# Kernel tuning notes

Hardware: AMD Instinct MI355X
Metric: run time of the kernel (lower is better)

## Reference

```python
import jax, jax.numpy as jnp
import numpy as np

B, S, D = 32, 1, 2048
H, KVH, HD = 16, 4, 128
MAXS = 4096
EPS = 1e-5
NREP = H // KVH  # GQA repeat factor = 4
FF = 4 * D
POS = 4095  # decode position (start_pos)


def setup_inputs() -> dict:
    key = jax.random.key(0)
    ks = jax.random.split(key, 12)
    sc = lambda d: 1.0 / np.sqrt(d)
    # RoPE angles for the current token position, [S, HD//2]
    inv_freq = 1.0 / (10000.0 ** (np.arange(0, HD, 2, dtype=np.float32) / HD))
    ang = (POS + np.arange(S, dtype=np.float32))[:, None] * inv_freq[None, :]
    return {
        "x": jax.random.normal(ks[0], (B, S, D), jnp.float32),
        "cos": jnp.asarray(np.cos(ang), jnp.float32),
        "sin": jnp.asarray(np.sin(ang), jnp.float32),
        "k_cache": jax.random.normal(ks[1], (B, MAXS, KVH, HD), jnp.float32),
        "v_cache": jax.random.normal(ks[2], (B, MAXS, KVH, HD), jnp.float32),
        "w_rms_attn": jnp.ones((D,), jnp.float32),
        "wq": jax.random.normal(ks[3], (D, D), jnp.float32) * sc(D),
        "wk": jax.random.normal(ks[4], (D, KVH * HD), jnp.float32) * sc(D),
        "wv": jax.random.normal(ks[5], (D, KVH * HD), jnp.float32) * sc(D),
        "wo": jax.random.normal(ks[6], (D, D), jnp.float32) * sc(D),
        "w_rms_ffn": jnp.ones((D,), jnp.float32),
        "w1": jax.random.normal(ks[7], (D, FF), jnp.float32) * sc(D),
        "w2": jax.random.normal(ks[8], (D, FF), jnp.float32) * sc(D),
        "w3": jax.random.normal(ks[9], (FF, D), jnp.float32) * sc(FF),
        "start_pos": POS,
    }


def _rmsnorm(x, g):
    return x * g * jax.lax.rsqrt(jnp.mean(x * x, axis=-1, keepdims=True) + EPS)


def _rope(x, cos, sin):
    # x: [B, S, h, HD]; complex rotation on (even, odd) pairs
    xr = x.reshape(*x.shape[:-1], HD // 2, 2)
    x0, x1 = xr[..., 0], xr[..., 1]
    c = cos[None, :, None, :]
    s = sin[None, :, None, :]
    r0 = x0 * c - x1 * s
    r1 = x0 * s + x1 * c
    return jnp.stack([r0, r1], axis=-1).reshape(x.shape)


def reference(x, cos, sin, k_cache, v_cache, w_rms_attn, wq, wk, wv, wo,
              w_rms_ffn, w1, w2, w3, start_pos):
    xa = _rmsnorm(x, w_rms_attn)
    xq = (xa @ wq).reshape(B, S, H, HD)
    xk = (xa @ wk).reshape(B, S, KVH, HD)
    xv = (xa @ wv).reshape(B, S, KVH, HD)
    # Source applies RoPE to K and V (not Q) -- reproduced faithfully.
    xk = _rope(xk, cos, sin)
    xv = _rope(xv, cos, sin)
    kc = jax.lax.dynamic_update_slice(k_cache, xk, (0, start_pos, 0, 0))
    vc = jax.lax.dynamic_update_slice(v_cache, xv, (0, start_pos, 0, 0))
    klen = start_pos + S
    keys = jnp.repeat(kc[:, :klen], NREP, axis=2)   # [B, klen, H, HD]
    vals = jnp.repeat(vc[:, :klen], NREP, axis=2)
    att = jnp.einsum('bqhd,bkhd->bhqk', xq, keys) * (HD ** -0.5)
    att = jax.nn.softmax(att, axis=-1)
    y = jnp.einsum('bhqk,bkhd->bqhd', att, vals).reshape(B, S, D)
    h = x + y @ wo
    xf = _rmsnorm(h, w_rms_ffn)
    return h + (jax.nn.silu(xf @ w1) * (xf @ w2)) @ w3
```

## Files before the change

kernel.cpp:

```cpp
#include <hip/hip_runtime.h>
#include <math.h>

#define BB 32
#define DD 2048
#define NKVH 4
#define HDIM 128
#define MAXS 4096
#define FFD 8192
#define POS 4095
#define EPSV 1e-5f
#define SCALE 0.08838834764831845f
#define ASPLIT 32
#define SPOS 128

#define OFF_QT   0u
#define OFF_KT   65536u
#define OFF_VT   81920u
#define OFF_G1   98304u
#define OFF_G2   360448u
#define ZERO_N   622592u
#define OFF_XAT  622592u
#define OFF_RK   688128u
#define OFF_RV   704512u
#define OFF_PML  720896u
#define OFF_PACC 753664u
#define OFF_YT   2850816u
#define OFF_H    2916352u
#define OFF_XFT  2981888u

#define REP32(M) M(0) M(1) M(2) M(3) M(4) M(5) M(6) M(7) M(8) M(9) M(10) M(11) M(12) M(13) M(14) M(15) M(16) M(17) M(18) M(19) M(20) M(21) M(22) M(23) M(24) M(25) M(26) M(27) M(28) M(29) M(30) M(31)
#define REP32A(M,X) M(0,X) M(1,X) M(2,X) M(3,X) M(4,X) M(5,X) M(6,X) M(7,X) M(8,X) M(9,X) M(10,X) M(11,X) M(12,X) M(13,X) M(14,X) M(15,X) M(16,X) M(17,X) M(18,X) M(19,X) M(20,X) M(21,X) M(22,X) M(23,X) M(24,X) M(25,X) M(26,X) M(27,X) M(28,X) M(29,X) M(30,X) M(31,X)

#define DECLA(i) float a##i = 0.f;
#define FMA1(i,k) a##i = fmaf(ap[(k)*32 + (i)], w##k, a##i);
#define STORET(i) tl[i] = a##i;
#define ATOMN(i) atomicAdd(C + (size_t)(i)*N + n, a##i);

template<int N, int CH, bool TOUT>
__device__ __forceinline__ void gemv_body(const float* __restrict__ At,
                                          const float* __restrict__ W,
                                          float* __restrict__ C, int colblk,
                                          float* tile) {
    int tid = (int)threadIdx.x;
    int n = colblk * 256 + tid;
    int d0 = blockIdx.y * CH;
    const float* Wp = W + (size_t)d0 * N + n;
    const float* ap = At + (size_t)d0 * 32;
    REP32(DECLA)
#pragma unroll 4
    for (int dd = 0; dd < CH; dd += 4) {
        float w0 = Wp[0];
        float w1 = Wp[(size_t)N];
        float w2 = Wp[(size_t)N * 2];
        float w3 = Wp[(size_t)N * 3];
        REP32A(FMA1, 0)
        REP32A(FMA1, 1)
        REP32A(FMA1, 2)
        REP32A(FMA1, 3)
        Wp += (size_t)N * 4;
        ap += 128;
    }
    if constexpr (TOUT) {
        float* tl = tile + tid * 33;
        REP32(STORET)
        __syncthreads();
        float* cb = C + (size_t)colblk * 256 * 32;
#pragma unroll
        for (int i = 0; i < 32; ++i) {
            int f = i * 256 + tid;
            atomicAdd(cb + f, tile[(f >> 5) * 33 + (f & 31)]);
        }
    } else {
        REP32(ATOMN)
    }
}

template<int N, int CH, bool TOUT>
__global__ __launch_bounds__(256) void gemv32_kernel(const float* __restrict__ At,
                                                     const float* __restrict__ W,
                                                     float* __restrict__ C) {
    if constexpr (TOUT) {
        __shared__ float tile[256 * 33];
        gemv_body<N, CH, true>(At, W, C, blockIdx.x, tile);
    } else {
        gemv_body<N, CH, false>(At, W, C, blockIdx.x, nullptr);
    }
}

template<int N, int CH, int HALF>
__global__ __launch_bounds__(256) void gemv32_dual_kernel(const float* __restrict__ At,
        const float* __restrict__ W0, const float* __restrict__ W1,
        float* __restrict__ C0, float* __restrict__ C1) {
    __shared__ float tile[256 * 33];
    int bx = blockIdx.x;
    if (bx < HALF) gemv_body<N, CH, true>(At, W0, C0, bx, tile);
    else           gemv_body<N, CH, true>(At, W1, C1, bx - HALF, tile);
}

__global__ void zero_kernel(float* __restrict__ p) {
    p[blockIdx.x * 256 + threadIdx.x] = 0.f;
}

__global__ void rmsnorm_kernel(const float* __restrict__ in, const float* __restrict__ g,
                               float* __restrict__ outT, float* __restrict__ cpy) {
    int b = blockIdx.x;
    int tid = threadIdx.x;
    const float* row = in + b * DD;
    float v[8];
    float ss = 0.f;
#pragma unroll
    for (int i = 0; i < 8; ++i) { v[i] = row[tid + i * 256]; ss += v[i] * v[i]; }
#pragma unroll
    for (int off = 32; off; off >>= 1) ss += __shfl_xor(ss, off);
    __shared__ float red[4];
    if ((tid & 63) == 0) red[tid >> 6] = ss;
    __syncthreads();
    ss = red[0] + red[1] + red[2] + red[3];
    float scale = rsqrtf(ss * (1.f / DD) + EPSV);
#pragma unroll
    for (int i = 0; i < 8; ++i) {
        int idx = tid + i * 256;
        outT[(size_t)idx * 32 + b] = v[i] * g[idx] * scale;
        if (cpy) cpy[b * DD + idx] = v[i];
    }
}

__global__ void rope_kernel(const float* __restrict__ kT, const float* __restrict__ vT,
                            const float* __restrict__ cosb, const float* __restrict__ sinb,
                            float* __restrict__ rk, float* __restrict__ rv) {
    int idx = blockIdx.x * 256 + threadIdx.x;
    int b = idx >> 8, rem = idx & 255;
    int kvh = rem >> 6, i = rem & 63;
    float c = cosb[i], s = sinb[i];
    int col = kvh * HDIM + 2 * i;
    float k0 = kT[(size_t)col * 32 + b], k1 = kT[(size_t)(col + 1) * 32 + b];
    float v0 = vT[(size_t)col * 32 + b], v1 = vT[(size_t)(col + 1) * 32 + b];
    int o = (b * NKVH + kvh) * HDIM + 2 * i;
    rk[o] = k0 * c - k1 * s; rk[o + 1] = k0 * s + k1 * c;
    rv[o] = v0 * c - v1 * s; rv[o + 1] = v0 * s + v1 * c;
}

__global__ __launch_bounds__(256) void attn_partial_kernel(
    const float* __restrict__ qT, const float* __restrict__ kc, const float* __restrict__ vc,
    const float* __restrict__ rk, const float* __restrict__ rv,
    float* __restrict__ pml, float* __restrict__ pacc) {
    int bid = blockIdx.x;
    int split = bid & 31, b = bid >> 5;
    int tid = threadIdx.x;
    int kvh = (tid >> 5) & 3;
    int c = tid & 31;
    int hi = tid >> 7;
    __shared__ float p_s[16][SPOS];
    __shared__ float red[128][17];

    float4 q4[4];
#pragma unroll
    for (int h = 0; h < 4; ++h) {
        int col = (kvh * 4 + h) * HDIM + c * 4;
        q4[h].x = qT[(size_t)(col + 0) * 32 + b];
        q4[h].y = qT[(size_t)(col + 1) * 32 + b];
        q4[h].z = qT[(size_t)(col + 2) * 32 + b];
        q4[h].w = qT[(size_t)(col + 3) * 32 + b];
    }
    int t0 = split * SPOS;
    const float* kbase = kc + (size_t)(b * MAXS + t0) * (NKVH * HDIM);
    const float* vbase = vc + (size_t)(b * MAXS + t0) * (NKVH * HDIM);

#define QK_BODY(SRC, POSL)                                                      \
    {                                                                           \
        float4 kk = *(const float4*)(SRC);                                      \
        float r0 = kk.x * q4[0].x + kk.y * q4[0].y + kk.z * q4[0].z + kk.w * q4[0].w; \
        float r1 = kk.x * q4[1].x + kk.y * q4[1].y + kk.z * q4[1].z + kk.w * q4[1].w; \
        float r2 = kk.x * q4[2].x + kk.y * q4[2].y + kk.z * q4[2].z + kk.w * q4[2].w; \
        float r3 = kk.x * q4[3].x + kk.y * q4[3].y + kk.z * q4[3].z + kk.w * q4[3].w; \
        _Pragma("unroll")                                                       \
        for (int m = 1; m < 32; m <<= 1) {                                      \
            r0 += __shfl_xor(r0, m); r1 += __shfl_xor(r1, m);                   \
            r2 += __shfl_xor(r2, m); r3 += __shfl_xor(r3, m);                   \
        }                                                                       \
        if (c == 0) {                                                           \
            p_s[kvh * 4 + 0][POSL] = r0 * SCALE;                                \
            p_s[kvh * 4 + 1][POSL] = r1 * SCALE;                                \
            p_s[kvh * 4 + 2][POSL] = r2 * SCALE;                                \
            p_s[kvh * 4 + 3][POSL] = r3 * SCALE;                                \
        }                                                                       \
    }

#pragma unroll 8
    for (int iter = 0; iter < 63; ++iter) {
        QK_BODY(kbase + iter * 1024 + tid * 4, iter * 2 + hi)
    }
    {
        int posl = 126 + hi;
        const float* src = (t0 + posl == POS)
            ? rk + (size_t)(b * NKVH + kvh) * HDIM + c * 4
            : kbase + 63 * 1024 + tid * 4;
        QK_BODY(src, posl)
    }
    __syncthreads();

    {
        int w = tid >> 6, lane = tid & 63;
#pragma unroll
        for (int hh = 0; hh < 4; ++hh) {
            int h = w * 4 + hh;
            float e0 = p_s[h][lane], e1 = p_s[h][lane + 64];
            float m = fmaxf(e0, e1);
#pragma unroll
            for (int off = 32; off; off >>= 1) m = fmaxf(m, __shfl_xor(m, off));
            e0 = __expf(e0 - m); e1 = __expf(e1 - m);
            p_s[h][lane] = e0; p_s[h][lane + 64] = e1;
            float l = e0 + e1;
#pragma unroll
            for (int off = 32; off; off >>= 1) l += __shfl_xor(l, off);
            if (lane == 0) {
                int idx = ((b * ASPLIT + split) * 16 + h) * 2;
                pml[idx] = m; pml[idx + 1] = l;
            }
        }
    }
    __syncthreads();

    float4 a0 = {0, 0, 0, 0}, a1 = a0, a2 = a0, a3 = a0;
#define PV_BODY(SRC, POSL)                                                      \
    {                                                                           \
        float4 vv = *(const float4*)(SRC);                                      \
        float p0 = p_s[kvh * 4 + 0][POSL], p1 = p_s[kvh * 4 + 1][POSL];         \
        float p2 = p_s[kvh * 4 + 2][POSL], p3 = p_s[kvh * 4 + 3][POSL];         \
        a0.x = fmaf(p0, vv.x, a0.x); a0.y = fmaf(p0, vv.y, a0.y);               \
        a0.z = fmaf(p0, vv.z, a0.z); a0.w = fmaf(p0, vv.w, a0.w);               \
        a1.x = fmaf(p1, vv.x, a1.x); a1.y = fmaf(p1, vv.y, a1.y);               \
        a1.z = fmaf(p1, vv.z, a1.z); a1.w = fmaf(p1, vv.w, a1.w);               \
        a2.x = fmaf(p2, vv.x, a2.x); a2.y = fmaf(p2, vv.y, a2.y);               \
        a2.z = fmaf(p2, vv.z, a2.z); a2.w = fmaf(p2, vv.w, a2.w);               \
        a3.x = fmaf(p3, vv.x, a3.x); a3.y = fmaf(p3, vv.y, a3.y);               \
        a3.z = fmaf(p3, vv.z, a3.z); a3.w = fmaf(p3, vv.w, a3.w);               \
    }
#pragma unroll 8
    for (int iter = 0; iter < 63; ++iter) {
        PV_BODY(vbase + iter * 1024 + tid * 4, iter * 2 + hi)
    }
    {
        int posl = 126 + hi;
        const float* src = (t0 + posl == POS)
            ? rv + (size_t)(b * NKVH + kvh) * HDIM + c * 4
            : vbase + 63 * 1024 + tid * 4;
        PV_BODY(src, posl)
    }
    if (tid >= 128) {
        float* r = &red[tid - 128][0];
        *(float4*)(r + 0) = a0; *(float4*)(r + 4) = a1;
        *(float4*)(r + 8) = a2; *(float4*)(r + 12) = a3;
    }
    __syncthreads();
    if (tid < 128) {
        const float* r = &red[tid][0];
        a0.x += r[0];  a0.y += r[1];  a0.z += r[2];  a0.w += r[3];
        a1.x += r[4];  a1.y += r[5];  a1.z += r[6];  a1.w += r[7];
        a2.x += r[8];  a2.y += r[9];  a2.z += r[10]; a2.w += r[11];
        a3.x += r[12]; a3.y += r[13]; a3.z += r[14]; a3.w += r[15];
        size_t base = ((size_t)(b * ASPLIT + split) * 16 + kvh * 4) * HDIM + c * 4;
        *(float4*)(pacc + base + 0 * HDIM) = a0;
        *(float4*)(pacc + base + 1 * HDIM) = a1;
        *(float4*)(pacc + base + 2 * HDIM) = a2;
        *(float4*)(pacc + base + 3 * HDIM) = a3;
    }
}

__global__ void attn_combine_kernel(const float* __restrict__ pml,
                                    const float* __restrict__ pacc, float* __restrict__ yT) {
    int bid = blockIdx.x;
    int b = bid >> 4, h = bid & 15;
    int d = threadIdx.x;
    float M = -INFINITY;
#pragma unroll 8
    for (int s = 0; s < ASPLIT; ++s)
        M = fmaxf(M, pml[((b * ASPLIT + s) * 16 + h) * 2]);
    float denom = 0.f, acc = 0.f;
#pragma unroll 4
    for (int s = 0; s < ASPLIT; ++s) {
        int idx = (b * ASPLIT + s) * 16 + h;
        float e = __expf(pml[idx * 2] - M);
        denom += pml[idx * 2 + 1] * e;
        acc += e * pacc[(size_t)idx * HDIM + d];
    }
    yT[(size_t)(h * HDIM + d) * 32 + b] = acc / denom;
}

__global__ void silu_mul_kernel(float* __restrict__ g1, const float* __restrict__ g2) {
    int i = blockIdx.x * 256 + threadIdx.x;
    float a = g1[i], bb = g2[i];
    g1[i] = a * bb / (1.f + __expf(-a));
}

extern "C" void kernel_launch(void* const* d_in, const int* in_sizes, int n_in,
                              void* d_out, int out_size, void* d_ws, size_t ws_size,
                              hipStream_t stream) {
    (void)in_sizes; (void)n_in; (void)out_size; (void)ws_size;
    const float* x    = (const float*)d_in[0];
    const float* cosb = (const float*)d_in[1];
    const float* sinb = (const float*)d_in[2];
    const float* kc   = (const float*)d_in[3];
    const float* vc   = (const float*)d_in[4];
    const float* wra  = (const float*)d_in[5];
    const float* wq   = (const float*)d_in[6];
    const float* wk   = (const float*)d_in[7];
    const float* wv   = (const float*)d_in[8];
    const float* wo   = (const float*)d_in[9];
    const float* wrf  = (const float*)d_in[10];
    const float* w1   = (const float*)d_in[11];
    const float* w2   = (const float*)d_in[12];
    const float* w3   = (const float*)d_in[13];
    float* out = (float*)d_out;
    float* ws  = (float*)d_ws;

    float* qT   = ws + OFF_QT;
    float* kT   = ws + OFF_KT;
    float* vT   = ws + OFF_VT;
    float* g1T  = ws + OFF_G1;
    float* g2T  = ws + OFF_G2;
    float* xaT  = ws + OFF_XAT;
    float* rk   = ws + OFF_RK;
    float* rv   = ws + OFF_RV;
    float* pml  = ws + OFF_PML;
    float* pacc = ws + OFF_PACC;
    float* yT   = ws + OFF_YT;
    float* h    = ws + OFF_H;
    float* xfT  = ws + OFF_XFT;

    zero_kernel<<<ZERO_N / 256, 256, 0, stream>>>(ws);

    rmsnorm_kernel<<<32, 256, 0, stream>>>(x, wra, xaT, h);
    gemv32_kernel<2048, 32, true><<<dim3(8, 64), 256, 0, stream>>>(xaT, wq, qT);
    gemv32_dual_kernel<512, 32, 2><<<dim3(4, 64), 256, 0, stream>>>(xaT, wk, wv, kT, vT);
    rope_kernel<<<32, 256, 0, stream>>>(kT, vT, cosb, sinb, rk, rv);
    attn_partial_kernel<<<1024, 256, 0, stream>>>(qT, kc, vc, rk, rv, pml, pacc);
    attn_combine_kernel<<<512, 128, 0, stream>>>(pml, pacc, yT);
    gemv32_kernel<2048, 32, false><<<dim3(8, 64), 256, 0, stream>>>(yT, wo, h);
    rmsnorm_kernel<<<32, 256, 0, stream>>>(h, wrf, xfT, out);
    gemv32_dual_kernel<8192, 128, 32><<<dim3(64, 16), 256, 0, stream>>>(xfT, w1, w2, g1T, g2T);
    silu_mul_kernel<<<1024, 256, 0, stream>>>(g1T, g2T);
    gemv32_kernel<2048, 128, false><<<dim3(8, 64), 256, 0, stream>>>(g1T, w3, out);
}
```

Baseline: 337.1 us.

## Stage KV cache tiles into LDS with async double-buffered loads in attention

```diff
diff --git a/kernel.cpp b/kernel.cpp
--- a/kernel.cpp
+++ b/kernel.cpp
@@ -27,6 +27,14 @@
 #define OFF_YT   2850816u
 #define OFF_H    2916352u
 #define OFF_XFT  2981888u
+#define OFF_KFIX 3047424u
+#define OFF_VFIX 3309568u
+
+#define VM_WAIT8 asm volatile("s_waitcnt vmcnt(8)" ::: "memory")
+#define VM_WAIT0 asm volatile("s_waitcnt vmcnt(0)" ::: "memory")
+#define LG_WAIT0 asm volatile("s_waitcnt lgkmcnt(0)" ::: "memory")
+#define SCHED0   __builtin_amdgcn_sched_barrier(0)
+#define SBAR     __builtin_amdgcn_s_barrier()
 
 #define REP32(M) M(0) M(1) M(2) M(3) M(4) M(5) M(6) M(7) M(8) M(9) M(10) M(11) M(12) M(13) M(14) M(15) M(16) M(17) M(18) M(19) M(20) M(21) M(22) M(23) M(24) M(25) M(26) M(27) M(28) M(29) M(30) M(31)
 #define REP32A(M,X) M(0,X) M(1,X) M(2,X) M(3,X) M(4,X) M(5,X) M(6,X) M(7,X) M(8,X) M(9,X) M(10,X) M(11,X) M(12,X) M(13,X) M(14,X) M(15,X) M(16,X) M(17,X) M(18,X) M(19,X) M(20,X) M(21,X) M(22,X) M(23,X) M(24,X) M(25,X) M(26,X) M(27,X) M(28,X) M(29,X) M(30,X) M(31,X)
@@ -140,131 +148,116 @@
     rv[o] = v0 * c - v1 * s; rv[o + 1] = v0 * s + v1 * c;
 }
 
-__global__ __launch_bounds__(256) void attn_partial_kernel(
-    const float* __restrict__ qT, const float* __restrict__ kc, const float* __restrict__ vc,
-    const float* __restrict__ rk, const float* __restrict__ rv,
+__global__ void fixlast_kernel(const float* __restrict__ kc, const float* __restrict__ vc,
+                               const float* __restrict__ rk, const float* __restrict__ rv,
+                               float* __restrict__ kfix, float* __restrict__ vfix) {
+    int idx = blockIdx.x * 256 + threadIdx.x;
+    int b = idx >> 13, rem = idx & 8191;
+    int pos = rem >> 9, col = rem & 511;
+    int gpos = 4080 + pos;
+    float kv, vv;
+    if (gpos == POS) {
+        kv = rk[b * 512 + col]; vv = rv[b * 512 + col];
+    } else {
+        size_t o = ((size_t)(b * MAXS + gpos)) * 512 + col;
+        kv = kc[o]; vv = vc[o];
+    }
+    kfix[idx] = kv; vfix[idx] = vv;
+}
+
+__global__ __launch_bounds__(256, 2) void attn_stage_kernel(
+    const float* __restrict__ qn, const float* __restrict__ kc, const float* __restrict__ vc,
+    const float* __restrict__ kfix, const float* __restrict__ vfix,
     float* __restrict__ pml, float* __restrict__ pacc) {
-    int bid = blockIdx.x;
-    int split = bid & 31, b = bid >> 5;
-    int tid = threadIdx.x;
-    int kvh = (tid >> 5) & 3;
-    int c = tid & 31;
-    int hi = tid >> 7;
-    __shared__ float p_s[16][SPOS];
-    __shared__ float red[128][17];
-
-    float4 q4[4];
-#pragma unroll
-    for (int h = 0; h < 4; ++h) {
-        int col = (kvh * 4 + h) * HDIM + c * 4;
-        q4[h].x = qT[(size_t)(col + 0) * 32 + b];
-        q4[h].y = qT[(size_t)(col + 1) * 32 + b];
-        q4[h].z = qT[(size_t)(col + 2) * 32 + b];
-        q4[h].w = qT[(size_t)(col + 3) * 32 + b];
-    }
+    int split = blockIdx.x & 31, b = blockIdx.x >> 5;
+    int tid = threadIdx.x, lane = tid & 63, wv = tid >> 6;
+    __shared__ float kbuf[2][8192];
+    __shared__ float p_s[128][16];
+    int qpos = tid >> 4, qhead = tid & 15;
+    int qr = qpos * 4 + (qhead >> 2);
+    int vh = tid >> 4, c16 = tid & 15, vkvh = vh >> 2;
     int t0 = split * SPOS;
-    const float* kbase = kc + (size_t)(b * MAXS + t0) * (NKVH * HDIM);
-    const float* vbase = vc + (size_t)(b * MAXS + t0) * (NKVH * HDIM);
-
-#define QK_BODY(SRC, POSL)                                                      \
-    {                                                                           \
-        float4 kk = *(const float4*)(SRC);                                      \
-        float r0 = kk.x * q4[0].x + kk.y * q4[0].y + kk.z * q4[0].z + kk.w * q4[0].w; \
-        float r1 = kk.x * q4[1].x + kk.y * q4[1].y + kk.z * q4[1].z + kk.w * q4[1].w; \
-        float r2 = kk.x * q4[2].x + kk.y * q4[2].y + kk.z * q4[2].z + kk.w * q4[2].w; \
-        float r3 = kk.x * q4[3].x + kk.y * q4[3].y + kk.z * q4[3].z + kk.w * q4[3].w; \
-        _Pragma("unroll")                                                       \
-        for (int m = 1; m < 32; m <<= 1) {                                      \
-            r0 += __shfl_xor(r0, m); r1 += __shfl_xor(r1, m);                   \
-            r2 += __shfl_xor(r2, m); r3 += __shfl_xor(r3, m);                   \
-        }                                                                       \
-        if (c == 0) {                                                           \
-            p_s[kvh * 4 + 0][POSL] = r0 * SCALE;                                \
-            p_s[kvh * 4 + 1][POSL] = r1 * SCALE;                                \
-            p_s[kvh * 4 + 2][POSL] = r2 * SCALE;                                \
-            p_s[kvh * 4 + 3][POSL] = r3 * SCALE;                                \
-        }                                                                       \
-    }
-
-#pragma unroll 8
-    for (int iter = 0; iter < 63; ++iter) {
-        QK_BODY(kbase + iter * 1024 + tid * 4, iter * 2 + hi)
-    }
-    {
-        int posl = 126 + hi;
-        const float* src = (t0 + posl == POS)
-            ? rk + (size_t)(b * NKVH + kvh) * HDIM + c * 4
-            : kbase + 63 * 1024 + tid * 4;
-        QK_BODY(src, posl)
-    }
-    __syncthreads();
-
-    {
-        int w = tid >> 6, lane = tid & 63;
-#pragma unroll
-        for (int hh = 0; hh < 4; ++hh) {
-            int h = w * 4 + hh;
-            float e0 = p_s[h][lane], e1 = p_s[h][lane + 64];
-            float m = fmaxf(e0, e1);
-#pragma unroll
-            for (int off = 32; off; off >>= 1) m = fmaxf(m, __shfl_xor(m, off));
-            e0 = __expf(e0 - m); e1 = __expf(e1 - m);
-            p_s[h][lane] = e0; p_s[h][lane + 64] = e1;
-            float l = e0 + e1;
-#pragma unroll
-            for (int off = 32; off; off >>= 1) l += __shfl_xor(l, off);
-            if (lane == 0) {
-                int idx = ((b * ASPLIT + split) * 16 + h) * 2;
-                pml[idx] = m; pml[idx + 1] = l;
+
+    float4 qrot[32];
+#pragma unroll
+    for (int j = 0; j < 32; ++j) {
+        int g = (j + qr) & 31;
+        qrot[j] = *(const float4*)(qn + (size_t)b * DD + qhead * HDIM + g * 4);
+    }
+    float4 av0 = {0, 0, 0, 0}, av1 = {0, 0, 0, 0};
+
+    auto stage = [&](int t) {
+        int s = t & 7;
+        const float* base;
+        if (t < 8) base = (split == 31 && s == 7) ? kfix + (size_t)b * 8192
+                                                  : kc + ((size_t)b * MAXS + t0 + s * 16) * 512;
+        else       base = (split == 31 && s == 7) ? vfix + (size_t)b * 8192
+                                                  : vc + ((size_t)b * MAXS + t0 + s * 16) * 512;
+        const float* g = base + wv * 2048 + lane * 4;
+        float* l = &kbuf[t & 1][wv * 2048];
+#pragma unroll
+        for (int i = 0; i < 8; ++i)
+            __builtin_amdgcn_global_load_lds(
+                (const __attribute__((address_space(1))) void*)(g + i * 256),
+                (__attribute__((address_space(3))) void*)(l + i * 256), 16, 0, 0);
+    };
+
+    stage(0);
+    for (int t = 0; t < 16; ++t) {
+        if (t < 15) { stage(t + 1); VM_WAIT8; } else { VM_WAIT0; }
+        SCHED0; SBAR;
+        if (t == 8) {
+#pragma unroll
+            for (int hh = 0; hh < 4; ++hh) {
+                int h = wv * 4 + hh;
+                float e0 = p_s[lane][h], e1 = p_s[lane + 64][h];
+                float m = fmaxf(e0, e1);
+#pragma unroll
+                for (int off = 32; off; off >>= 1) m = fmaxf(m, __shfl_xor(m, off));
+                e0 = __expf(e0 - m); e1 = __expf(e1 - m);
+                p_s[lane][h] = e0; p_s[lane + 64][h] = e1;
+                float l2 = e0 + e1;
+#pragma unroll
+                for (int off = 32; off; off >>= 1) l2 += __shfl_xor(l2, off);
+                if (lane == 0) {
+                    int idx = ((b * ASPLIT + split) * 16 + h) * 2;
+                    pml[idx] = m; pml[idx + 1] = l2;
+                }
             }
         }
-    }
-    __syncthreads();
-
-    float4 a0 = {0, 0, 0, 0}, a1 = a0, a2 = a0, a3 = a0;
-#define PV_BODY(SRC, POSL)                                                      \
-    {                                                                           \
-        float4 vv = *(const float4*)(SRC);                                      \
-        float p0 = p_s[kvh * 4 + 0][POSL], p1 = p_s[kvh * 4 + 1][POSL];         \
-        float p2 = p_s[kvh * 4 + 2][POSL], p3 = p_s[kvh * 4 + 3][POSL];         \
-        a0.x = fmaf(p0, vv.x, a0.x); a0.y = fmaf(p0, vv.y, a0.y);               \
-        a0.z = fmaf(p0, vv.z, a0.z); a0.w = fmaf(p0, vv.w, a0.w);               \
-        a1.x = fmaf(p1, vv.x, a1.x); a1.y = fmaf(p1, vv.y, a1.y);               \
-        a1.z = fmaf(p1, vv.z, a1.z); a1.w = fmaf(p1, vv.w, a1.w);               \
-        a2.x = fmaf(p2, vv.x, a2.x); a2.y = fmaf(p2, vv.y, a2.y);               \
-        a2.z = fmaf(p2, vv.z, a2.z); a2.w = fmaf(p2, vv.w, a2.w);               \
-        a3.x = fmaf(p3, vv.x, a3.x); a3.y = fmaf(p3, vv.y, a3.y);               \
-        a3.z = fmaf(p3, vv.z, a3.z); a3.w = fmaf(p3, vv.w, a3.w);               \
-    }
-#pragma unroll 8
-    for (int iter = 0; iter < 63; ++iter) {
-        PV_BODY(vbase + iter * 1024 + tid * 4, iter * 2 + hi)
-    }
-    {
-        int posl = 126 + hi;
-        const float* src = (t0 + posl == POS)
-            ? rv + (size_t)(b * NKVH + kvh) * HDIM + c * 4
-            : vbase + 63 * 1024 + tid * 4;
-        PV_BODY(src, posl)
-    }
-    if (tid >= 128) {
-        float* r = &red[tid - 128][0];
-        *(float4*)(r + 0) = a0; *(float4*)(r + 4) = a1;
-        *(float4*)(r + 8) = a2; *(float4*)(r + 12) = a3;
-    }
-    __syncthreads();
-    if (tid < 128) {
-        const float* r = &red[tid][0];
-        a0.x += r[0];  a0.y += r[1];  a0.z += r[2];  a0.w += r[3];
-        a1.x += r[4];  a1.y += r[5];  a1.z += r[6];  a1.w += r[7];
-        a2.x += r[8];  a2.y += r[9];  a2.z += r[10]; a2.w += r[11];
-        a3.x += r[12]; a3.y += r[13]; a3.z += r[14]; a3.w += r[15];
-        size_t base = ((size_t)(b * ASPLIT + split) * 16 + kvh * 4) * HDIM + c * 4;
-        *(float4*)(pacc + base + 0 * HDIM) = a0;
-        *(float4*)(pacc + base + 1 * HDIM) = a1;
-        *(float4*)(pacc + base + 2 * HDIM) = a2;
-        *(float4*)(pacc + base + 3 * HDIM) = a3;
-    }
+        const float* kb = kbuf[t & 1];
+        if (t < 8) {
+            float4 acc = {0, 0, 0, 0};
+            const float* rowp = kb + qr * 128;
+#pragma unroll
+            for (int j = 0; j < 32; ++j) {
+                int g = (j + qr) & 31;
+                float4 k4 = *(const float4*)(rowp + g * 4);
+                acc.x = fmaf(k4.x, qrot[j].x, acc.x);
+                acc.y = fmaf(k4.y, qrot[j].y, acc.y);
+                acc.z = fmaf(k4.z, qrot[j].z, acc.z);
+                acc.w = fmaf(k4.w, qrot[j].w, acc.w);
+            }
+            p_s[t * 16 + qpos][qhead] = (acc.x + acc.y + acc.z + acc.w) * SCALE;
+        } else {
+            int s = t - 8;
+            const float* vrow = kb + vkvh * 128 + c16 * 4;
+#pragma unroll
+            for (int p = 0; p < 16; ++p) {
+                float pw = p_s[s * 16 + p][vh];
+                float4 v0 = *(const float4*)(vrow + p * 512);
+                float4 v1 = *(const float4*)(vrow + p * 512 + 64);
+                av0.x = fmaf(pw, v0.x, av0.x); av0.y = fmaf(pw, v0.y, av0.y);
+                av0.z = fmaf(pw, v0.z, av0.z); av0.w = fmaf(pw, v0.w, av0.w);
+                av1.x = fmaf(pw, v1.x, av1.x); av1.y = fmaf(pw, v1.y, av1.y);
+                av1.z = fmaf(pw, v1.z, av1.z); av1.w = fmaf(pw, v1.w, av1.w);
+            }
+        }
+        LG_WAIT0; SCHED0; SBAR;
+    }
+    size_t pbase = ((size_t)(b * ASPLIT + split) * 16 + vh) * HDIM;
+    *(float4*)(pacc + pbase + c16 * 4) = av0;
+    *(float4*)(pacc + pbase + 64 + c16 * 4) = av1;
 }
 
 __global__ void attn_combine_kernel(const float* __restrict__ pml,
@@ -314,7 +307,7 @@
     float* out = (float*)d_out;
     float* ws  = (float*)d_ws;
 
-    float* qT   = ws + OFF_QT;
+    float* qn   = ws + OFF_QT;
     float* kT   = ws + OFF_KT;
     float* vT   = ws + OFF_VT;
     float* g1T  = ws + OFF_G1;
@@ -327,14 +320,17 @@
     float* yT   = ws + OFF_YT;
     float* h    = ws + OFF_H;
     float* xfT  = ws + OFF_XFT;
+    float* kfix = ws + OFF_KFIX;
+    float* vfix = ws + OFF_VFIX;
 
     zero_kernel<<<ZERO_N / 256, 256, 0, stream>>>(ws);
 
     rmsnorm_kernel<<<32, 256, 0, stream>>>(x, wra, xaT, h);
-    gemv32_kernel<2048, 32, true><<<dim3(8, 64), 256, 0, stream>>>(xaT, wq, qT);
+    gemv32_kernel<2048, 32, false><<<dim3(8, 64), 256, 0, stream>>>(xaT, wq, qn);
     gemv32_dual_kernel<512, 32, 2><<<dim3(4, 64), 256, 0, stream>>>(xaT, wk, wv, kT, vT);
     rope_kernel<<<32, 256, 0, stream>>>(kT, vT, cosb, sinb, rk, rv);
-    attn_partial_kernel<<<1024, 256, 0, stream>>>(qT, kc, vc, rk, rv, pml, pacc);
+    fixlast_kernel<<<1024, 256, 0, stream>>>(kc, vc, rk, rv, kfix, vfix);
+    attn_stage_kernel<<<1024, 256, 0, stream>>>(qn, kc, vc, kfix, vfix, pml, pacc);
     attn_combine_kernel<<<512, 128, 0, stream>>>(pml, pacc, yT);
     gemv32_kernel<2048, 32, false><<<dim3(8, 64), 256, 0, stream>>>(yT, wo, h);
     rmsnorm_kernel<<<32, 256, 0, stream>>>(h, wrf, xfT, out);
```

Result: faster. 309.7 us (-8.1%).
